# Optimization experiments

Measured on AMD Instinct MI355X. Metric: run time of the kernel, lower is better.

Reference implementation:

```python
import jax, jax.numpy as jnp
import numpy as np

# static configuration (matches init_kwargs)
CTX = 512   # context_dim
D = 512     # d_model
H = 8       # nhead
HD = D // H
L = 4       # num_layers
FF = 2048   # dim_feedforward
P = 24      # prediction_length
TS = 1      # time_series_dim
B = 256     # batch size
NEG = -1e9  # additive mask value (== -inf after softmax in fp32)


def _pos_encoding():
    pos = np.arange(P, dtype=np.float32)[:, None]
    div = np.exp(np.arange(0, D, 2, dtype=np.float32) * (-np.log(10000.0) / D))
    pe = np.zeros((P, D), dtype=np.float32)
    pe[:, 0::2] = np.sin(pos * div)
    pe[:, 1::2] = np.cos(pos * div)
    return jnp.asarray(pe[:, None, :])  # [P, 1, D] (seq-first broadcast over batch)


def setup_inputs() -> dict:
    key = jax.random.key(0)
    ks = iter(jax.random.split(key, 64))
    def g(shape, scale=0.02):
        return jax.random.normal(next(ks), shape, dtype=jnp.float32) * scale
    return {
        "context": jax.random.normal(next(ks), (B, CTX), dtype=jnp.float32),
        "start_token": g((1, 1, TS), 1.0),
        "ctx_W": g((D, CTX)), "ctx_b": jnp.zeros((D,), jnp.float32),
        "ve_W": g((D, TS)),   "ve_b": jnp.zeros((D,), jnp.float32),
        "sa_in_w": g((L, 3 * D, D)), "sa_in_b": jnp.zeros((L, 3 * D), jnp.float32),
        "sa_out_w": g((L, D, D)),    "sa_out_b": jnp.zeros((L, D), jnp.float32),
        "ca_in_w": g((L, 3 * D, D)), "ca_in_b": jnp.zeros((L, 3 * D), jnp.float32),
        "ca_out_w": g((L, D, D)),    "ca_out_b": jnp.zeros((L, D), jnp.float32),
        "lin1_w": g((L, FF, D)), "lin1_b": jnp.zeros((L, FF), jnp.float32),
        "lin2_w": g((L, D, FF)), "lin2_b": jnp.zeros((L, D), jnp.float32),
        "ln1_w": jnp.ones((L, D), jnp.float32), "ln1_b": jnp.zeros((L, D), jnp.float32),
        "ln2_w": jnp.ones((L, D), jnp.float32), "ln2_b": jnp.zeros((L, D), jnp.float32),
        "ln3_w": jnp.ones((L, D), jnp.float32), "ln3_b": jnp.zeros((L, D), jnp.float32),
        "o1_w": g((D // 2, D)), "o1_b": jnp.zeros((D // 2,), jnp.float32),
        "o2_w": g((TS, D // 2)), "o2_b": jnp.zeros((TS,), jnp.float32),
    }


def _layer_norm(x, w, b, eps=1e-5):
    m = jnp.mean(x, -1, keepdims=True)
    v = jnp.mean(jnp.square(x - m), -1, keepdims=True)
    return (x - m) / jnp.sqrt(v + eps) * w + b


def _mha(q_in, kv_in, in_w, in_b, out_w, out_b, mask):
    # q_in: [S,B,D] seq-first, kv_in: [T,B,D]
    Wq, Wk, Wv = jnp.split(in_w, 3, axis=0)
    bq, bk, bv = jnp.split(in_b, 3)
    S = q_in.shape[0]; T = kv_in.shape[0]
    q = (q_in @ Wq.T + bq).reshape(S, -1, H, HD)
    k = (kv_in @ Wk.T + bk).reshape(T, -1, H, HD)
    v = (kv_in @ Wv.T + bv).reshape(T, -1, H, HD)
    scores = jnp.einsum('sbhd,tbhd->bhst', q, k) / np.sqrt(HD).astype(np.float32)
    if mask is not None:
        scores = scores + mask
    attn = jax.nn.softmax(scores, axis=-1)
    o = jnp.einsum('bhst,tbhd->sbhd', attn, v).reshape(S, -1, D)
    return o @ out_w.T + out_b


def reference(context, start_token, ctx_W, ctx_b, ve_W, ve_b,
              sa_in_w, sa_in_b, sa_out_w, sa_out_b,
              ca_in_w, ca_in_b, ca_out_w, ca_out_b,
              lin1_w, lin1_b, lin2_w, lin2_b,
              ln1_w, ln1_b, ln2_w, ln2_b, ln3_w, ln3_b,
              o1_w, o1_b, o2_w, o2_b):
    pe = _pos_encoding()
    causal = jnp.where(jnp.tril(jnp.ones((P, P), bool)), 0.0, NEG)[None, None]  # [1,1,P,P]
    memory = (context @ ctx_W.T + ctx_b)[None]  # [1,B,D]

    def decode(vals):
        # vals: [P+1,B,TS]; only the first P slots form the (padded) target sequence.
        # Causal mask guarantees position t only sees slots <= t, so reading
        # position t reproduces the original length-(t+1) decode exactly.
        x = vals[:P] @ ve_W.T + ve_b + pe  # [P,B,D]
        for i in range(L):
            sa = _mha(x, x, sa_in_w[i], sa_in_b[i], sa_out_w[i], sa_out_b[i], causal)
            x = _layer_norm(x + sa, ln1_w[i], ln1_b[i])
            ca = _mha(x, memory, ca_in_w[i], ca_in_b[i], ca_out_w[i], ca_out_b[i], None)
            x = _layer_norm(x + ca, ln2_w[i], ln2_b[i])
            h = jax.nn.gelu(x @ lin1_w[i].T + lin1_b[i], approximate=False)
            x = _layer_norm(x + h @ lin2_w[i].T + lin2_b[i], ln3_w[i], ln3_b[i])
        return x

    def step(vals, t):
        x = decode(vals)
        last = jnp.take(x, t, axis=0)  # [B,D] output at current last position
        h = jax.nn.gelu(last @ o1_w.T + o1_b, approximate=False)
        nv = h @ o2_w.T + o2_b  # [B,TS]
        vals = jax.lax.dynamic_update_slice(vals, nv[None], (t + 1, 0, 0))
        return vals, nv

    vals0 = jnp.zeros((P + 1, B, TS), jnp.float32)
    vals0 = vals0.at[0].set(jnp.broadcast_to(start_token[0, 0], (B, TS)))
    _, ys = jax.lax.scan(jax.checkpoint(step), vals0, jnp.arange(P))
    return jnp.transpose(ys, (1, 0, 2))  # [B,P,TS]
```

## Files before the change

kernel.cpp:

```cpp
#include <hip/hip_runtime.h>
#include <math.h>


#define B    256
#define D    512
#define H    8
#define HD   64
#define L    4
#define FF   2048
#define P    24
#define NBLK 256
#define NTHR 512
#define NGRP 8
#define GSZ  32
#define CS   ((size_t)B * H * P * HD)

struct MegaArgs {
  const float *context, *start_token, *ctx_W, *ctx_b, *ve_W, *ve_b;
  const float *sa_in_w, *sa_in_b, *sa_out_w, *sa_out_b;
  const float *ca_in_w, *ca_in_b, *ca_out_w, *ca_out_b;
  const float *lin1_w, *lin1_b, *lin2_w, *lin2_b;
  const float *ln1_w, *ln1_b, *ln2_w, *ln2_b, *ln3_w, *ln3_b;
  const float *o1_w, *o1_b, *o2_w, *o2_b;
  float *out;
  float *pe, *vals, *memory, *ca_add, *x, *qbuf, *hbuf, *part, *hh,
        *kcache, *vcache;
};

__device__ __forceinline__ float gld(const float* p)
{
  return __hip_atomic_load((float*)p, __ATOMIC_RELAXED,
                           __HIP_MEMORY_SCOPE_AGENT);
}
__device__ __forceinline__ void gst(float* p, float v)
{
  __hip_atomic_store(p, v, __ATOMIC_RELAXED, __HIP_MEMORY_SCOPE_AGENT);
}

__device__ __align__(128) unsigned g_cnt[NGRP * 32];
__device__ __align__(128) unsigned g_root = 0;
__device__ __align__(128) unsigned g_gen  = 0;
__device__ __align__(128) unsigned g_base = 0;

__device__ __forceinline__ void grid_bar(unsigned &bno)
{
  ++bno;
  __syncthreads();
  if (threadIdx.x == 0) {
    unsigned* cnt = &g_cnt[(blockIdx.x & (NGRP - 1)) * 32];
    const unsigned o = __hip_atomic_fetch_add(cnt, 1u, __ATOMIC_RELAXED,
                                              __HIP_MEMORY_SCOPE_AGENT);
    if (o == bno * GSZ - 1u) {
      const unsigned r = __hip_atomic_fetch_add(&g_root, 1u, __ATOMIC_RELAXED,
                                                __HIP_MEMORY_SCOPE_AGENT);
      if (r == bno * NGRP - 1u)
        __hip_atomic_store(&g_gen, bno, __ATOMIC_RELAXED,
                           __HIP_MEMORY_SCOPE_AGENT);
    }
    while (__hip_atomic_load(&g_gen, __ATOMIC_RELAXED,
                             __HIP_MEMORY_SCOPE_AGENT) < bno)
      __builtin_amdgcn_s_sleep(4);
  }
  __syncthreads();
}

__device__ __forceinline__ float gelu_f(float v)
{
  return 0.5f * v * (1.0f + erff(v * 0.70710678118654752f));
}

template <int LOADER, int EPI>
__device__ void gemmK(float* sh,
                      const float* A, int lda,
                      const float* W, int ldw, const float* bias,
                      float* C, int ldc, int m0, int n0, int k0, int KL,
                      float* kcp, float* vcp, int t,
                      const float* valst, const float* veW, const float* veb,
                      const float* pet, float* xout)
{
  float* As = sh;
  float* Ws = sh + 16 * 68;
  const int tid = threadIdx.x;
  const int c  = tid & 15;
  const int r  = tid >> 4;
  const int tm = tid >> 4;
  const int tn = tid & 15;

  float vv0 = 0.f, vv1 = 0.f;
  if constexpr (LOADER == 1) {
    vv0 = gld(valst + m0 + r);
    vv1 = gld(valst + m0 + r + 32);
  }

  auto ldA = [&](int kb, int rr, float vv) -> float {
    const int k = k0 + kb + c;
    if constexpr (LOADER == 1) {
      const float av = vv * veW[k] + veb[k] + gld(pet + k);
      if (xout) gst(xout + (size_t)(m0 + rr) * D + k, av);
      return av;
    } else {
      return gld(A + (size_t)(m0 + rr) * lda + k);
    }
  };
  auto ldW = [&](int kb, int rr) -> float {
    return W[(size_t)(n0 + rr) * ldw + k0 + kb + c];
  };

  float a0 = ldA(0, r, vv0), a1 = ldA(0, r + 32, vv1);
  float w0 = ldW(0, r),      w1 = ldW(0, r + 32);
  float acc[2][4] = {};

  for (int kb = 0; kb < KL; kb += 16) {
    As[c * 68 + r]      = a0;
    As[c * 68 + r + 32] = a1;
    Ws[c * 68 + r]      = w0;
    Ws[c * 68 + r + 32] = w1;
    __syncthreads();
    if (kb + 16 < KL) {
      a0 = ldA(kb + 16, r, vv0); a1 = ldA(kb + 16, r + 32, vv1);
      w0 = ldW(kb + 16, r);      w1 = ldW(kb + 16, r + 32);
    }
#pragma unroll
    for (int kk = 0; kk < 16; kk++) {
      const float2 a2 = *(const float2*)(As + kk * 68 + tm * 2);
      const float4 w4 = *(const float4*)(Ws + kk * 68 + tn * 4);
      acc[0][0] = fmaf(a2.x, w4.x, acc[0][0]);
      acc[0][1] = fmaf(a2.x, w4.y, acc[0][1]);
      acc[0][2] = fmaf(a2.x, w4.z, acc[0][2]);
      acc[0][3] = fmaf(a2.x, w4.w, acc[0][3]);
      acc[1][0] = fmaf(a2.y, w4.x, acc[1][0]);
      acc[1][1] = fmaf(a2.y, w4.y, acc[1][1]);
      acc[1][2] = fmaf(a2.y, w4.z, acc[1][2]);
      acc[1][3] = fmaf(a2.y, w4.w, acc[1][3]);
    }
    __syncthreads();
  }

#pragma unroll
  for (int i = 0; i < 2; i++) {
    const int m = m0 + tm * 2 + i;
#pragma unroll
    for (int j = 0; j < 4; j++) {
      const int n = n0 + tn * 4 + j;
      float v = acc[i][j];
      if constexpr (EPI != 3) v += bias[n];
      if constexpr (EPI == 1) v = gelu_f(v);
      if constexpr (EPI == 2) {
        if (n < D) {
          gst(C + (size_t)m * D + n, v);
        } else if (n < 2 * D) {
          const int f = n - D;
          gst(kcp + ((size_t)(m * H + (f >> 6)) * P + t) * HD + (f & 63), v);
        } else {
          const int f = n - 2 * D;
          gst(vcp + ((size_t)(m * H + (f >> 6)) * P + t) * HD + (f & 63), v);
        }
      } else {
        gst(C + (size_t)m * ldc + n, v);
      }
    }
  }
}

__device__ __forceinline__ float rsum512(float v, float* sbf)
{
#pragma unroll
  for (int o = 32; o; o >>= 1) v += __shfl_xor(v, o);
  const int wid = threadIdx.x >> 6;
  if ((threadIdx.x & 63) == 0) sbf[wid] = v;
  __syncthreads();
  float s = 0.f;
#pragma unroll
  for (int w = 0; w < 8; w++) s += sbf[w];
  __syncthreads();
  return s;
}

__global__ __launch_bounds__(NTHR) void mega(MegaArgs a)
{
  __shared__ float sh[2 * 16 * 68];
  __shared__ float sbf[8];
  const int blk = blockIdx.x;
  unsigned bno = __hip_atomic_load(&g_base, __ATOMIC_RELAXED,
                                   __HIP_MEMORY_SCOPE_AGENT);
  float* attn_o = a.part + (size_t)4 * B * D;

  if (blk < 32) {
    gemmK<0, 0>(sh, a.context, D, a.ctx_W, D, a.ctx_b, a.memory, D,
                (blk & 3) * 64, (blk >> 2) * 64, 0, 512,
                nullptr, nullptr, 0, nullptr, nullptr, nullptr, nullptr,
                nullptr);
  } else if (blk < 56) {
    const int tt = blk - 32;
    const int dd = threadIdx.x;
    const float fr = expf((float)(dd & ~1) * (-9.210340371976184f / (float)D));
    const float ang = (float)tt * fr;
    gst(a.pe + tt * D + dd, (dd & 1) ? cosf(ang) : sinf(ang));
  } else if (blk == 56) {
    if (threadIdx.x < B) gst(a.vals + threadIdx.x, a.start_token[0]);
  }
  grid_bar(bno);

  if (blk < 128) {
    const int l = blk >> 5, tile = blk & 31;
    gemmK<0, 0>(sh, a.memory, D,
                a.ca_in_w + (size_t)l * 3 * D * D + (size_t)2 * D * D, D,
                a.ca_in_b + l * 3 * D + 2 * D,
                a.part + (size_t)l * B * D, D,
                (tile & 3) * 64, (tile >> 2) * 64, 0, 512,
                nullptr, nullptr, 0, nullptr, nullptr, nullptr, nullptr,
                nullptr);
  }
  grid_bar(bno);

  if (blk < 128) {
    const int l = blk >> 5, tile = blk & 31;
    gemmK<0, 0>(sh, a.part + (size_t)l * B * D, D,
                a.ca_out_w + (size_t)l * D * D, D, a.ca_out_b + l * D,
                a.ca_add + (size_t)l * B * D, D,
                (tile & 3) * 64, (tile >> 2) * 64, 0, 512,
                nullptr, nullptr, 0, nullptr, nullptr, nullptr, nullptr,
                nullptr);
  }
  grid_bar(bno);

  for (int t = 0; t < P; t++) {
    for (int l = 0; l < L; l++) {
      float* kcp = a.kcache + (size_t)l * CS;
      float* vcp = a.vcache + (size_t)l * CS;

      if (blk < 96) {
        const int m0 = (blk & 3) * 64, n0 = (blk >> 2) * 64;
        if (l == 0)
          gemmK<1, 2>(sh, nullptr, 0, a.sa_in_w, D, a.sa_in_b, a.qbuf, D,
                      m0, n0, 0, 512, kcp, vcp, t,
                      a.vals + (size_t)t * B, a.ve_W, a.ve_b, a.pe + t * D,
                      (n0 == 0) ? a.x : nullptr);
        else
          gemmK<0, 2>(sh, a.x, D, a.sa_in_w + (size_t)l * 3 * D * D, D,
                      a.sa_in_b + l * 3 * D, a.qbuf, D, m0, n0, 0, 512,
                      kcp, vcp, t, nullptr, nullptr, nullptr, nullptr,
                      nullptr);
      }
      grid_bar(bno);

      {
        const int wid = threadIdx.x >> 6, lane = threadIdx.x & 63;
        const int u = blk * 8 + wid;
        const int b = u >> 3, h = u & 7;
        const float q = gld(a.qbuf + (size_t)b * D + h * HD + lane);
        const float* kb = kcp + (size_t)(b * H + h) * P * HD;
        const float* vb = vcp + (size_t)(b * H + h) * P * HD;
        float sc[P];
        const int nn = t + 1;
#pragma unroll
        for (int j = 0; j < P; j++)
          if (j < nn) {
            float p = q * gld(kb + j * HD + lane);
#pragma unroll
            for (int o = 32; o; o >>= 1) p += __shfl_xor(p, o);
            sc[j] = p * 0.125f;
          }
        float mx = -1e30f;
#pragma unroll
        for (int j = 0; j < P; j++)
          if (j < nn) mx = fmaxf(mx, sc[j]);
        float s = 0.f;
#pragma unroll
        for (int j = 0; j < P; j++)
          if (j < nn) { sc[j] = expf(sc[j] - mx); s += sc[j]; }
        const float inv = 1.0f / s;
        float o = 0.f;
#pragma unroll
        for (int j = 0; j < P; j++)
          if (j < nn) o = fmaf(sc[j], gld(vb + j * HD + lane), o);
        gst(attn_o + (size_t)b * D + h * HD + lane, o * inv);
      }
      grid_bar(bno);

      if (blk < 128) {
        const int kc = blk >> 5, tile = blk & 31;
        gemmK<0, 3>(sh, attn_o, D, a.sa_out_w + (size_t)l * D * D, D,
                    nullptr, a.part + (size_t)kc * B * D, D,
                    (tile & 3) * 64, (tile >> 2) * 64, kc * 128, 128,
                    nullptr, nullptr, 0, nullptr, nullptr, nullptr, nullptr,
                    nullptr);
      }
      grid_bar(bno);

      {
        const int b = blk, dd = threadIdx.x;
        const size_t o = (size_t)b * D + dd;
        float u = gld(a.x + o) + a.sa_out_b[l * D + dd];
#pragma unroll
        for (int kc = 0; kc < 4; kc++)
          u += gld(a.part + (size_t)kc * B * D + o);
        const float m1 = rsum512(u, sbf) * (1.0f / D);
        const float d1 = u - m1;
        const float v1 = rsum512(d1 * d1, sbf) * (1.0f / D);
        const float z = d1 * rsqrtf(v1 + 1e-5f) * a.ln1_w[l * D + dd]
                        + a.ln1_b[l * D + dd];
        const float r2 = z + gld(a.ca_add + (size_t)l * B * D + o);
        const float m2 = rsum512(r2, sbf) * (1.0f / D);
        const float d2 = r2 - m2;
        const float v2 = rsum512(d2 * d2, sbf) * (1.0f / D);
        gst(a.x + o, d2 * rsqrtf(v2 + 1e-5f) * a.ln2_w[l * D + dd]
                     + a.ln2_b[l * D + dd]);
      }
      grid_bar(bno);

      if (blk < 128)
        gemmK<0, 1>(sh, a.x, D, a.lin1_w + (size_t)l * FF * D, D,
                    a.lin1_b + l * FF, a.hbuf, FF,
                    (blk & 3) * 64, (blk >> 2) * 64, 0, 512,
                    nullptr, nullptr, 0, nullptr, nullptr, nullptr, nullptr,
                    nullptr);
      grid_bar(bno);

      {
        const int kc = blk >> 5, tile = blk & 31;
        gemmK<0, 3>(sh, a.hbuf, FF, a.lin2_w + (size_t)l * D * FF, FF,
                    nullptr, a.part + (size_t)kc * B * D, D,
                    (tile & 3) * 64, (tile >> 2) * 64, kc * 256, 256,
                    nullptr, nullptr, 0, nullptr, nullptr, nullptr, nullptr,
                    nullptr);
      }
      grid_bar(bno);

      {
        const int b = blk, dd = threadIdx.x;
        const size_t o = (size_t)b * D + dd;
        float s0 = gld(a.x + o) + a.lin2_b[l * D + dd];
#pragma unroll
        for (int kc = 0; kc < 8; kc++)
          s0 += gld(a.part + (size_t)kc * B * D + o);
        const float m1 = rsum512(s0, sbf) * (1.0f / D);
        const float d1 = s0 - m1;
        const float v1 = rsum512(d1 * d1, sbf) * (1.0f / D);
        gst(a.x + o, d1 * rsqrtf(v1 + 1e-5f) * a.ln3_w[l * D + dd]
                     + a.ln3_b[l * D + dd]);
      }
      grid_bar(bno);
    }

    if (blk < 16)
      gemmK<0, 1>(sh, a.x, D, a.o1_w, D, a.o1_b, a.hh, 256,
                  (blk & 3) * 64, (blk >> 2) * 64, 0, 512,
                  nullptr, nullptr, 0, nullptr, nullptr, nullptr, nullptr,
                  nullptr);
    grid_bar(bno);

    if (blk < 32) {
      const int wid = threadIdx.x >> 6, lane = threadIdx.x & 63;
      const int r = blk * 8 + wid;
      float p = 0.f;
#pragma unroll
      for (int i = 0; i < 4; i++)
        p = fmaf(gld(a.hh + (size_t)r * 256 + lane + i * 64),
                 a.o2_w[lane + i * 64], p);
#pragma unroll
      for (int o = 32; o; o >>= 1) p += __shfl_xor(p, o);
      if (lane == 0) {
        const float v = p + a.o2_b[0];
        gst(a.vals + (size_t)(t + 1) * B + r, v);
        a.out[(size_t)r * P + t] = v;
      }
    }
    grid_bar(bno);
  }

  if (blk == 0 && threadIdx.x == 0)
    __hip_atomic_store(&g_base, bno, __ATOMIC_RELAXED,
                       __HIP_MEMORY_SCOPE_AGENT);
}

extern "C" void kernel_launch(void* const* d_in, const int* in_sizes, int n_in,
                              void* d_out, int out_size, void* d_ws,
                              size_t ws_size, hipStream_t stream)
{
  (void)in_sizes; (void)n_in; (void)out_size; (void)ws_size;
  MegaArgs h;
  h.context     = (const float*)d_in[0];
  h.start_token = (const float*)d_in[1];
  h.ctx_W  = (const float*)d_in[2];
  h.ctx_b  = (const float*)d_in[3];
  h.ve_W   = (const float*)d_in[4];
  h.ve_b   = (const float*)d_in[5];
  h.sa_in_w  = (const float*)d_in[6];
  h.sa_in_b  = (const float*)d_in[7];
  h.sa_out_w = (const float*)d_in[8];
  h.sa_out_b = (const float*)d_in[9];
  h.ca_in_w  = (const float*)d_in[10];
  h.ca_in_b  = (const float*)d_in[11];
  h.ca_out_w = (const float*)d_in[12];
  h.ca_out_b = (const float*)d_in[13];
  h.lin1_w = (const float*)d_in[14];
  h.lin1_b = (const float*)d_in[15];
  h.lin2_w = (const float*)d_in[16];
  h.lin2_b = (const float*)d_in[17];
  h.ln1_w = (const float*)d_in[18];
  h.ln1_b = (const float*)d_in[19];
  h.ln2_w = (const float*)d_in[20];
  h.ln2_b = (const float*)d_in[21];
  h.ln3_w = (const float*)d_in[22];
  h.ln3_b = (const float*)d_in[23];
  h.o1_w = (const float*)d_in[24];
  h.o1_b = (const float*)d_in[25];
  h.o2_w = (const float*)d_in[26];
  h.o2_b = (const float*)d_in[27];
  h.out = (float*)d_out;

  float* ws = (float*)d_ws;
  size_t off = 0;
  h.pe      = ws + off; off += (size_t)P * D;
  h.vals    = ws + off; off += (size_t)(P + 1) * B;
  h.memory  = ws + off; off += (size_t)B * D;
  h.ca_add  = ws + off; off += (size_t)L * B * D;
  h.x       = ws + off; off += (size_t)B * D;
  h.qbuf    = ws + off; off += (size_t)B * D;
  h.hbuf    = ws + off; off += (size_t)B * FF;
  h.part    = ws + off; off += (size_t)8 * B * D;
  h.hh      = ws + off; off += (size_t)B * 256;
  h.kcache  = ws + off; off += (size_t)L * CS;
  h.vcache  = ws + off; off += (size_t)L * CS;

  void* kargs[] = { &h };
  hipLaunchCooperativeKernel(mega, dim3(NBLK), dim3(NTHR), kargs, 0, stream);
}
```

Measured before the change: 12.76 ms.

## Vectorize global accesses, restructure attention and layernorm, remap GEMM tiles

Replaces scalar atomic loads and stores with dwordx4 vector loads and stores that carry cache-bypass bits. Attention is rewritten so each lane handles four head dims and four keys, and layernorm now handles four rows per block with float4 work. GEMM tiles are remapped across blocks, the register prefetch pipeline in the GEMM loader is dropped, layer 0 recomputes the embedding inside layernorm instead of writing x from the QKV GEMM, and the barrier spin sleep is shortened. Some plain (cached) loads of cross-block data such as vals, ca_add and the memory buffer now rely on the barrier's vmcnt wait for coherence, which risks stale reads.

```diff
diff --git a/kernel.cpp b/kernel.cpp
--- a/kernel.cpp
+++ b/kernel.cpp
@@ -15,6 +15,9 @@
 #define GSZ  32
 #define CS   ((size_t)B * H * P * HD)
 
+typedef float f4 __attribute__((ext_vector_type(4)));
+typedef float f2 __attribute__((ext_vector_type(2)));
+
 struct MegaArgs {
   const float *context, *start_token, *ctx_W, *ctx_b, *ve_W, *ve_b;
   const float *sa_in_w, *sa_in_b, *sa_out_w, *sa_out_b;
@@ -36,6 +39,19 @@
 {
   __hip_atomic_store(p, v, __ATOMIC_RELAXED, __HIP_MEMORY_SCOPE_AGENT);
 }
+__device__ __forceinline__ void gst4(float* p, f4 v)
+{
+  asm volatile("global_store_dwordx4 %0, %1, off sc0 sc1"
+               :: "v"(p), "v"(v) : "memory");
+}
+__device__ __forceinline__ f4 gld4e(const float* p)
+{
+  f4 r;
+  asm volatile("global_load_dwordx4 %0, %1, off sc0 sc1\n\t"
+               "s_waitcnt vmcnt(0)"
+               : "=&v"(r) : "v"(p) : "memory");
+  return r;
+}
 
 __device__ __align__(128) unsigned g_cnt[NGRP * 32];
 __device__ __align__(128) unsigned g_root = 0;
@@ -45,6 +61,7 @@
 __device__ __forceinline__ void grid_bar(unsigned &bno)
 {
   ++bno;
+  asm volatile("s_waitcnt vmcnt(0)" ::: "memory");
   __syncthreads();
   if (threadIdx.x == 0) {
     unsigned* cnt = &g_cnt[(blockIdx.x & (NGRP - 1)) * 32];
@@ -59,7 +76,7 @@
     }
     while (__hip_atomic_load(&g_gen, __ATOMIC_RELAXED,
                              __HIP_MEMORY_SCOPE_AGENT) < bno)
-      __builtin_amdgcn_s_sleep(4);
+      __builtin_amdgcn_s_sleep(2);
   }
   __syncthreads();
 }
@@ -67,6 +84,11 @@
 __device__ __forceinline__ float gelu_f(float v)
 {
   return 0.5f * v * (1.0f + erff(v * 0.70710678118654752f));
+}
+__device__ __forceinline__ f4 gelu4(f4 v)
+{
+  v.x = gelu_f(v.x); v.y = gelu_f(v.y); v.z = gelu_f(v.z); v.w = gelu_f(v.w);
+  return v;
 }
 
 template <int LOADER, int EPI>
@@ -76,54 +98,44 @@
                       float* C, int ldc, int m0, int n0, int k0, int KL,
                       float* kcp, float* vcp, int t,
                       const float* valst, const float* veW, const float* veb,
-                      const float* pet, float* xout)
+                      const float* pet)
 {
   float* As = sh;
   float* Ws = sh + 16 * 68;
   const int tid = threadIdx.x;
-  const int c  = tid & 15;
-  const int r  = tid >> 4;
   const int tm = tid >> 4;
   const int tn = tid & 15;
+  float acc[2][4] = {};
 
   float vv0 = 0.f, vv1 = 0.f;
   if constexpr (LOADER == 1) {
-    vv0 = gld(valst + m0 + r);
-    vv1 = gld(valst + m0 + r + 32);
-  }
-
-  auto ldA = [&](int kb, int rr, float vv) -> float {
-    const int k = k0 + kb + c;
-    if constexpr (LOADER == 1) {
-      const float av = vv * veW[k] + veb[k] + gld(pet + k);
-      if (xout) gst(xout + (size_t)(m0 + rr) * D + k, av);
-      return av;
-    } else {
-      return gld(A + (size_t)(m0 + rr) * lda + k);
-    }
-  };
-  auto ldW = [&](int kb, int rr) -> float {
-    return W[(size_t)(n0 + rr) * ldw + k0 + kb + c];
-  };
-
-  float a0 = ldA(0, r, vv0), a1 = ldA(0, r + 32, vv1);
-  float w0 = ldW(0, r),      w1 = ldW(0, r + 32);
-  float acc[2][4] = {};
+    vv0 = valst[m0 + (tid >> 4)];
+    vv1 = valst[m0 + 32 + (tid >> 4)];
+  }
 
   for (int kb = 0; kb < KL; kb += 16) {
-    As[c * 68 + r]      = a0;
-    As[c * 68 + r + 32] = a1;
-    Ws[c * 68 + r]      = w0;
-    Ws[c * 68 + r + 32] = w1;
+#pragma unroll
+    for (int i = 0; i < 2; i++) {
+      const int idx = tid + i * 512;
+      const int r = idx >> 4;
+      const int c = idx & 15;
+      const int k = k0 + kb + c;
+      float av;
+      if constexpr (LOADER == 1) {
+        av = (i ? vv1 : vv0) * veW[k] + veb[k] + pet[k];
+      } else if constexpr (LOADER == 2) {
+        av = A[(size_t)(m0 + r) * lda + k];
+      } else {
+        av = gld(A + (size_t)(m0 + r) * lda + k);
+      }
+      As[c * 68 + r] = av;
+      Ws[c * 68 + r] = W[(size_t)(n0 + r) * ldw + k];
+    }
     __syncthreads();
-    if (kb + 16 < KL) {
-      a0 = ldA(kb + 16, r, vv0); a1 = ldA(kb + 16, r + 32, vv1);
-      w0 = ldW(kb + 16, r);      w1 = ldW(kb + 16, r + 32);
-    }
 #pragma unroll
     for (int kk = 0; kk < 16; kk++) {
-      const float2 a2 = *(const float2*)(As + kk * 68 + tm * 2);
-      const float4 w4 = *(const float4*)(Ws + kk * 68 + tn * 4);
+      const f2 a2 = *(const f2*)(As + kk * 68 + tm * 2);
+      const f4 w4 = *(const f4*)(Ws + kk * 68 + tn * 4);
       acc[0][0] = fmaf(a2.x, w4.x, acc[0][0]);
       acc[0][1] = fmaf(a2.x, w4.y, acc[0][1]);
       acc[0][2] = fmaf(a2.x, w4.z, acc[0][2]);
@@ -136,45 +148,45 @@
     __syncthreads();
   }
 
+  const int n4 = n0 + tn * 4;
 #pragma unroll
   for (int i = 0; i < 2; i++) {
     const int m = m0 + tm * 2 + i;
-#pragma unroll
-    for (int j = 0; j < 4; j++) {
-      const int n = n0 + tn * 4 + j;
-      float v = acc[i][j];
-      if constexpr (EPI != 3) v += bias[n];
-      if constexpr (EPI == 1) v = gelu_f(v);
-      if constexpr (EPI == 2) {
-        if (n < D) {
-          gst(C + (size_t)m * D + n, v);
-        } else if (n < 2 * D) {
-          const int f = n - D;
-          gst(kcp + ((size_t)(m * H + (f >> 6)) * P + t) * HD + (f & 63), v);
-        } else {
-          const int f = n - 2 * D;
-          gst(vcp + ((size_t)(m * H + (f >> 6)) * P + t) * HD + (f & 63), v);
-        }
+    f4 v;
+    v.x = acc[i][0]; v.y = acc[i][1]; v.z = acc[i][2]; v.w = acc[i][3];
+    if constexpr (EPI != 3) v += *(const f4*)(bias + n4);
+    if constexpr (EPI == 1) v = gelu4(v);
+    if constexpr (EPI == 2) {
+      if (n4 < D) {
+        gst4(C + (size_t)m * D + n4, v);
+      } else if (n4 < 2 * D) {
+        const int f = n4 - D;
+        gst4(kcp + ((size_t)(m * H + (f >> 6)) * P + t) * HD + (f & 63), v);
       } else {
-        gst(C + (size_t)m * ldc + n, v);
-      }
-    }
-  }
-}
-
-__device__ __forceinline__ float rsum512(float v, float* sbf)
+        const int f = n4 - 2 * D;
+        gst4(vcp + ((size_t)(m * H + (f >> 6)) * P + t) * HD + (f & 63), v);
+      }
+    } else {
+      gst4(C + (size_t)m * ldc + n4, v);
+    }
+  }
+}
+
+__device__ __forceinline__ float rsum128(float v, float* sb)
 {
 #pragma unroll
   for (int o = 32; o; o >>= 1) v += __shfl_xor(v, o);
-  const int wid = threadIdx.x >> 6;
-  if ((threadIdx.x & 63) == 0) sbf[wid] = v;
+  const int w = threadIdx.x >> 6;
+  if ((threadIdx.x & 63) == 0) sb[w] = v;
   __syncthreads();
-  float s = 0.f;
-#pragma unroll
-  for (int w = 0; w < 8; w++) s += sbf[w];
+  const int rl = threadIdx.x >> 7;
+  const float s = sb[rl * 2] + sb[rl * 2 + 1];
   __syncthreads();
   return s;
 }
+
+#define NKMAP(b) ((((b) >> 5) << 3) | ((b) & 7))
+#define MMAP(b)  (((b) >> 3) & 3)
 
 __global__ __launch_bounds__(NTHR) void mega(MegaArgs a)
 {
@@ -186,10 +198,9 @@
   float* attn_o = a.part + (size_t)4 * B * D;
 
   if (blk < 32) {
-    gemmK<0, 0>(sh, a.context, D, a.ctx_W, D, a.ctx_b, a.memory, D,
+    gemmK<2, 0>(sh, a.context, 512, a.ctx_W, 512, a.ctx_b, a.memory, D,
                 (blk & 3) * 64, (blk >> 2) * 64, 0, 512,
-                nullptr, nullptr, 0, nullptr, nullptr, nullptr, nullptr,
-                nullptr);
+                nullptr, nullptr, 0, nullptr, nullptr, nullptr, nullptr);
   } else if (blk < 56) {
     const int tt = blk - 32;
     const int dd = threadIdx.x;
@@ -203,24 +214,22 @@
 
   if (blk < 128) {
     const int l = blk >> 5, tile = blk & 31;
-    gemmK<0, 0>(sh, a.memory, D,
+    gemmK<2, 0>(sh, a.memory, D,
                 a.ca_in_w + (size_t)l * 3 * D * D + (size_t)2 * D * D, D,
                 a.ca_in_b + l * 3 * D + 2 * D,
                 a.part + (size_t)l * B * D, D,
                 (tile & 3) * 64, (tile >> 2) * 64, 0, 512,
-                nullptr, nullptr, 0, nullptr, nullptr, nullptr, nullptr,
-                nullptr);
+                nullptr, nullptr, 0, nullptr, nullptr, nullptr, nullptr);
   }
   grid_bar(bno);
 
   if (blk < 128) {
     const int l = blk >> 5, tile = blk & 31;
-    gemmK<0, 0>(sh, a.part + (size_t)l * B * D, D,
+    gemmK<2, 0>(sh, a.part + (size_t)l * B * D, D,
                 a.ca_out_w + (size_t)l * D * D, D, a.ca_out_b + l * D,
                 a.ca_add + (size_t)l * B * D, D,
                 (tile & 3) * 64, (tile >> 2) * 64, 0, 512,
-                nullptr, nullptr, 0, nullptr, nullptr, nullptr, nullptr,
-                nullptr);
+                nullptr, nullptr, 0, nullptr, nullptr, nullptr, nullptr);
   }
   grid_bar(bno);
 
@@ -230,17 +239,16 @@
       float* vcp = a.vcache + (size_t)l * CS;
 
       if (blk < 96) {
-        const int m0 = (blk & 3) * 64, n0 = (blk >> 2) * 64;
+        const int m0 = MMAP(blk) * 64, n0 = NKMAP(blk) * 64;
         if (l == 0)
           gemmK<1, 2>(sh, nullptr, 0, a.sa_in_w, D, a.sa_in_b, a.qbuf, D,
                       m0, n0, 0, 512, kcp, vcp, t,
-                      a.vals + (size_t)t * B, a.ve_W, a.ve_b, a.pe + t * D,
-                      (n0 == 0) ? a.x : nullptr);
+                      a.vals + (size_t)t * B, a.ve_W, a.ve_b,
+                      a.pe + (size_t)t * D);
         else
           gemmK<0, 2>(sh, a.x, D, a.sa_in_w + (size_t)l * 3 * D * D, D,
                       a.sa_in_b + l * 3 * D, a.qbuf, D, m0, n0, 0, 512,
-                      kcp, vcp, t, nullptr, nullptr, nullptr, nullptr,
-                      nullptr);
+                      kcp, vcp, t, nullptr, nullptr, nullptr, nullptr);
       }
       grid_bar(bno);
 
@@ -248,97 +256,130 @@
         const int wid = threadIdx.x >> 6, lane = threadIdx.x & 63;
         const int u = blk * 8 + wid;
         const int b = u >> 3, h = u & 7;
-        const float q = gld(a.qbuf + (size_t)b * D + h * HD + lane);
+        const int g = lane >> 4;
+        const int hd0 = (lane & 15) * 4;
         const float* kb = kcp + (size_t)(b * H + h) * P * HD;
         const float* vb = vcp + (size_t)(b * H + h) * P * HD;
-        float sc[P];
+        const f4 q4 = gld4e(a.qbuf + (size_t)b * D + h * HD + hd0);
         const int nn = t + 1;
+        float p[6];
+#pragma unroll
+        for (int bt = 0; bt < 6; bt++) {
+          const int j = bt * 4 + g;
+          float s = -1e30f;
+          if (j < nn) {
+            const f4 k4 = *(const f4*)(kb + j * HD + hd0);
+            s = q4.x * k4.x + q4.y * k4.y + q4.z * k4.z + q4.w * k4.w;
+          }
+#pragma unroll
+          for (int o = 1; o <= 8; o <<= 1) s += __shfl_xor(s, o);
+          p[bt] = s * 0.125f;
+        }
+        float mx = -1e30f;
+#pragma unroll
+        for (int bt = 0; bt < 6; bt++)
+          if (bt * 4 + g < nn) mx = fmaxf(mx, p[bt]);
+        mx = fmaxf(mx, __shfl_xor(mx, 16));
+        mx = fmaxf(mx, __shfl_xor(mx, 32));
+        float sum = 0.f;
+#pragma unroll
+        for (int bt = 0; bt < 6; bt++) {
+          const int j = bt * 4 + g;
+          const float e = (j < nn) ? expf(p[bt] - mx) : 0.f;
+          p[bt] = e; sum += e;
+        }
+        sum += __shfl_xor(sum, 16);
+        sum += __shfl_xor(sum, 32);
+        const float inv = 1.0f / sum;
+        f4 o4 = {0.f, 0.f, 0.f, 0.f};
 #pragma unroll
         for (int j = 0; j < P; j++)
           if (j < nn) {
-            float p = q * gld(kb + j * HD + lane);
-#pragma unroll
-            for (int o = 32; o; o >>= 1) p += __shfl_xor(p, o);
-            sc[j] = p * 0.125f;
+            const float pj = __shfl(p[j >> 2], ((j & 3) << 4) | (lane & 15));
+            const f4 v4 = *(const f4*)(vb + j * HD + hd0);
+            o4 += (pj * inv) * v4;
           }
-        float mx = -1e30f;
-#pragma unroll
-        for (int j = 0; j < P; j++)
-          if (j < nn) mx = fmaxf(mx, sc[j]);
-        float s = 0.f;
-#pragma unroll
-        for (int j = 0; j < P; j++)
-          if (j < nn) { sc[j] = expf(sc[j] - mx); s += sc[j]; }
-        const float inv = 1.0f / s;
-        float o = 0.f;
-#pragma unroll
-        for (int j = 0; j < P; j++)
-          if (j < nn) o = fmaf(sc[j], gld(vb + j * HD + lane), o);
-        gst(attn_o + (size_t)b * D + h * HD + lane, o * inv);
+        gst4(attn_o + (size_t)b * D + h * HD + hd0, o4);
       }
       grid_bar(bno);
 
       if (blk < 128) {
-        const int kc = blk >> 5, tile = blk & 31;
+        const int nk = NKMAP(blk);
         gemmK<0, 3>(sh, attn_o, D, a.sa_out_w + (size_t)l * D * D, D,
-                    nullptr, a.part + (size_t)kc * B * D, D,
-                    (tile & 3) * 64, (tile >> 2) * 64, kc * 128, 128,
-                    nullptr, nullptr, 0, nullptr, nullptr, nullptr, nullptr,
-                    nullptr);
-      }
-      grid_bar(bno);
-
-      {
-        const int b = blk, dd = threadIdx.x;
-        const size_t o = (size_t)b * D + dd;
-        float u = gld(a.x + o) + a.sa_out_b[l * D + dd];
-#pragma unroll
-        for (int kc = 0; kc < 4; kc++)
-          u += gld(a.part + (size_t)kc * B * D + o);
-        const float m1 = rsum512(u, sbf) * (1.0f / D);
-        const float d1 = u - m1;
-        const float v1 = rsum512(d1 * d1, sbf) * (1.0f / D);
-        const float z = d1 * rsqrtf(v1 + 1e-5f) * a.ln1_w[l * D + dd]
-                        + a.ln1_b[l * D + dd];
-        const float r2 = z + gld(a.ca_add + (size_t)l * B * D + o);
-        const float m2 = rsum512(r2, sbf) * (1.0f / D);
-        const float d2 = r2 - m2;
-        const float v2 = rsum512(d2 * d2, sbf) * (1.0f / D);
-        gst(a.x + o, d2 * rsqrtf(v2 + 1e-5f) * a.ln2_w[l * D + dd]
-                     + a.ln2_b[l * D + dd]);
+                    nullptr, a.part + (size_t)(nk >> 3) * B * D, D,
+                    MMAP(blk) * 64, (nk & 7) * 64, (nk >> 3) * 128, 128,
+                    nullptr, nullptr, 0, nullptr, nullptr, nullptr, nullptr);
+      }
+      grid_bar(bno);
+
+      if (blk < 64) {
+        const int row = blk * 4 + (threadIdx.x >> 7);
+        const int cc = (threadIdx.x & 127) * 4;
+        const size_t o = (size_t)row * D + cc;
+        f4 u;
+        if (l == 0) {
+          const float vv = a.vals[(size_t)t * B + row];
+          u = vv * (*(const f4*)(a.ve_W + cc)) + *(const f4*)(a.ve_b + cc)
+              + *(const f4*)(a.pe + (size_t)t * D + cc);
+        } else {
+          u = gld4e(a.x + o);
+        }
+        u += *(const f4*)(a.sa_out_b + l * D + cc);
+        u += gld4e(a.part + o);
+        u += gld4e(a.part + (size_t)B * D + o);
+        u += gld4e(a.part + (size_t)2 * B * D + o);
+        u += gld4e(a.part + (size_t)3 * B * D + o);
+        const float m1 = rsum128(u.x + u.y + u.z + u.w, sbf) * (1.0f / D);
+        f4 d = u - m1;
+        const float v1 =
+            rsum128(d.x * d.x + d.y * d.y + d.z * d.z + d.w * d.w, sbf)
+            * (1.0f / D);
+        f4 z = d * rsqrtf(v1 + 1e-5f) * (*(const f4*)(a.ln1_w + l * D + cc))
+               + *(const f4*)(a.ln1_b + l * D + cc);
+        f4 r2 = z + *(const f4*)(a.ca_add + (size_t)l * B * D + o);
+        const float m2 = rsum128(r2.x + r2.y + r2.z + r2.w, sbf) * (1.0f / D);
+        f4 d2 = r2 - m2;
+        const float v2 =
+            rsum128(d2.x * d2.x + d2.y * d2.y + d2.z * d2.z + d2.w * d2.w,
+                    sbf) * (1.0f / D);
+        f4 z2 = d2 * rsqrtf(v2 + 1e-5f) * (*(const f4*)(a.ln2_w + l * D + cc))
+                + *(const f4*)(a.ln2_b + l * D + cc);
+        gst4(a.x + o, z2);
       }
       grid_bar(bno);
 
       if (blk < 128)
         gemmK<0, 1>(sh, a.x, D, a.lin1_w + (size_t)l * FF * D, D,
                     a.lin1_b + l * FF, a.hbuf, FF,
-                    (blk & 3) * 64, (blk >> 2) * 64, 0, 512,
-                    nullptr, nullptr, 0, nullptr, nullptr, nullptr, nullptr,
-                    nullptr);
+                    MMAP(blk) * 64, NKMAP(blk) * 64, 0, 512,
+                    nullptr, nullptr, 0, nullptr, nullptr, nullptr, nullptr);
       grid_bar(bno);
 
       {
-        const int kc = blk >> 5, tile = blk & 31;
+        const int nk = NKMAP(blk);
         gemmK<0, 3>(sh, a.hbuf, FF, a.lin2_w + (size_t)l * D * FF, FF,
-                    nullptr, a.part + (size_t)kc * B * D, D,
-                    (tile & 3) * 64, (tile >> 2) * 64, kc * 256, 256,
-                    nullptr, nullptr, 0, nullptr, nullptr, nullptr, nullptr,
-                    nullptr);
-      }
-      grid_bar(bno);
-
-      {
-        const int b = blk, dd = threadIdx.x;
-        const size_t o = (size_t)b * D + dd;
-        float s0 = gld(a.x + o) + a.lin2_b[l * D + dd];
+                    nullptr, a.part + (size_t)(nk >> 3) * B * D, D,
+                    MMAP(blk) * 64, (nk & 7) * 64, (nk >> 3) * 256, 256,
+                    nullptr, nullptr, 0, nullptr, nullptr, nullptr, nullptr);
+      }
+      grid_bar(bno);
+
+      if (blk < 64) {
+        const int row = blk * 4 + (threadIdx.x >> 7);
+        const int cc = (threadIdx.x & 127) * 4;
+        const size_t o = (size_t)row * D + cc;
+        f4 s0 = gld4e(a.x + o) + *(const f4*)(a.lin2_b + l * D + cc);
 #pragma unroll
         for (int kc = 0; kc < 8; kc++)
-          s0 += gld(a.part + (size_t)kc * B * D + o);
-        const float m1 = rsum512(s0, sbf) * (1.0f / D);
-        const float d1 = s0 - m1;
-        const float v1 = rsum512(d1 * d1, sbf) * (1.0f / D);
-        gst(a.x + o, d1 * rsqrtf(v1 + 1e-5f) * a.ln3_w[l * D + dd]
-                     + a.ln3_b[l * D + dd]);
+          s0 += gld4e(a.part + (size_t)kc * B * D + o);
+        const float m1 = rsum128(s0.x + s0.y + s0.z + s0.w, sbf) * (1.0f / D);
+        f4 d = s0 - m1;
+        const float v1 =
+            rsum128(d.x * d.x + d.y * d.y + d.z * d.z + d.w * d.w, sbf)
+            * (1.0f / D);
+        f4 z = d * rsqrtf(v1 + 1e-5f) * (*(const f4*)(a.ln3_w + l * D + cc))
+               + *(const f4*)(a.ln3_b + l * D + cc);
+        gst4(a.x + o, z);
       }
       grid_bar(bno);
     }
@@ -346,22 +387,19 @@
     if (blk < 16)
       gemmK<0, 1>(sh, a.x, D, a.o1_w, D, a.o1_b, a.hh, 256,
                   (blk & 3) * 64, (blk >> 2) * 64, 0, 512,
-                  nullptr, nullptr, 0, nullptr, nullptr, nullptr, nullptr,
-                  nullptr);
+                  nullptr, nullptr, 0, nullptr, nullptr, nullptr, nullptr);
     grid_bar(bno);
 
     if (blk < 32) {
       const int wid = threadIdx.x >> 6, lane = threadIdx.x & 63;
       const int r = blk * 8 + wid;
-      float p = 0.f;
-#pragma unroll
-      for (int i = 0; i < 4; i++)
-        p = fmaf(gld(a.hh + (size_t)r * 256 + lane + i * 64),
-                 a.o2_w[lane + i * 64], p);
-#pragma unroll
-      for (int o = 32; o; o >>= 1) p += __shfl_xor(p, o);
+      const f4 hv = gld4e(a.hh + (size_t)r * 256 + lane * 4);
+      const f4 wv = *(const f4*)(a.o2_w + lane * 4);
+      float pp = hv.x * wv.x + hv.y * wv.y + hv.z * wv.z + hv.w * wv.w;
+#pragma unroll
+      for (int o = 32; o; o >>= 1) pp += __shfl_xor(pp, o);
       if (lane == 0) {
-        const float v = p + a.o2_b[0];
+        const float v = pp + a.o2_b[0];
         gst(a.vals + (size_t)(t + 1) * B + r, v);
         a.out[(size_t)r * P + t] = v;
       }
```

New measurement: 12.78 ms. Within noise of the previous version (+0.1%).
